# Optimization experiments

Hardware: AMD Instinct MI355X
Metric: run time of the kernel (lower is better)

Reference implementation:

```python
import jax, jax.numpy as jnp
import numpy as np

DIM = 1280
HEADS = 16
HEAD_DIM = DIM // HEADS  # 80
SEQ = 2048


def setup_inputs() -> dict:
    key = jax.random.key(0)
    ks = jax.random.split(key, 6)
    hidden_states = jax.random.normal(ks[0], (SEQ, DIM), jnp.float32)
    rotary_pos_emb = jax.random.normal(ks[1], (SEQ, HEAD_DIM // 2), jnp.float32)
    # 4 variable-length windows packed into one flat sequence
    cu_seqlens = jnp.array([0, 512, 1024, 1536, 2048], jnp.int32)
    w_scale = DIM ** -0.5
    qkv_w = jax.random.normal(ks[2], (3 * DIM, DIM), jnp.float32) * w_scale
    qkv_b = jax.random.normal(ks[3], (3 * DIM,), jnp.float32) * 0.01
    proj_w = jax.random.normal(ks[4], (DIM, DIM), jnp.float32) * w_scale
    proj_b = jax.random.normal(ks[5], (DIM,), jnp.float32) * 0.01
    return {
        "hidden_states": hidden_states,
        "rotary_pos_emb": rotary_pos_emb,
        "cu_seqlens": cu_seqlens,
        "qkv_w": qkv_w,
        "qkv_b": qkv_b,
        "proj_w": proj_w,
        "proj_b": proj_b,
    }


def _apply_rope_vision(x, freqs):
    # x: [S, H, D], freqs: [S, D//2]; matches Qwen2-VL apply_rotary_pos_emb_vision
    cos = jnp.concatenate([jnp.cos(freqs), jnp.cos(freqs)], axis=-1)[:, None, :]  # [S,1,D]
    sin = jnp.concatenate([jnp.sin(freqs), jnp.sin(freqs)], axis=-1)[:, None, :]
    x1, x2 = jnp.split(x, 2, axis=-1)
    rot = jnp.concatenate([-x2, x1], axis=-1)  # rotate_half
    return x * cos + rot * sin


def reference(hidden_states, rotary_pos_emb, cu_seqlens, qkv_w, qkv_b, proj_w, proj_b):
    S = hidden_states.shape[0]
    qkv = (hidden_states @ qkv_w.T + qkv_b).reshape(S, 3, HEADS, HEAD_DIM)
    q, k, v = qkv[:, 0], qkv[:, 1], qkv[:, 2]  # each [S, H, D]
    q = _apply_rope_vision(q, rotary_pos_emb)
    k = _apply_rope_vision(k, rotary_pos_emb)
    # varlen attention: tokens attend only within their cu_seqlens window
    seg = jnp.searchsorted(cu_seqlens[1:], jnp.arange(S), side="right")
    mask = seg[:, None] == seg[None, :]  # [S, S]
    scale = HEAD_DIM ** -0.5
    scores = jnp.einsum("shd,thd->hst", q, k) * scale  # [H, S, S]
    scores = jnp.where(mask[None, :, :], scores, jnp.finfo(scores.dtype).min)
    probs = jax.nn.softmax(scores, axis=-1)
    attn = jnp.einsum("hst,thd->shd", probs, v).reshape(S, DIM)
    return attn @ proj_w.T + proj_b
```

## Files before the change

kernel.cpp:

```cpp
#include <hip/hip_runtime.h>


typedef __attribute__((ext_vector_type(8))) short bf16x8;
typedef __attribute__((ext_vector_type(4))) float floatx4;
typedef __attribute__((ext_vector_type(4))) short short4v;
typedef __attribute__((ext_vector_type(8))) short short8v;

static __device__ __forceinline__ short f2bf(float f) {
  union { float f; unsigned u; } v; v.f = f;
  unsigned r = v.u + 0x7FFFu + ((v.u >> 16) & 1u);
  return (short)(r >> 16);
}
static __device__ __forceinline__ float bf2f(short h) {
  union { unsigned u; float f; } v;
  v.u = ((unsigned)(unsigned short)h) << 16;
  return v.f;
}

static __device__ __forceinline__ void gload16(const short* g, short* l) {
  __builtin_amdgcn_global_load_lds(
      (const __attribute__((address_space(1))) unsigned*)g,
      (__attribute__((address_space(3))) unsigned*)l, 16, 0, 0);
}

__global__ __launch_bounds__(256) void cvt_kernel(const float* __restrict__ src,
                                                  short* __restrict__ dst, int n8) {
  int i = blockIdx.x * 256 + threadIdx.x;
  if (i >= n8) return;
  float4 x = ((const float4*)src)[2 * i];
  float4 y = ((const float4*)src)[2 * i + 1];
  short8v o;
  o[0] = f2bf(x.x); o[1] = f2bf(x.y); o[2] = f2bf(x.z); o[3] = f2bf(x.w);
  o[4] = f2bf(y.x); o[5] = f2bf(y.y); o[6] = f2bf(y.z); o[7] = f2bf(y.w);
  ((short8v*)dst)[i] = o;
}

template <int MODE, int BM, int BN>
__global__ __launch_bounds__(256) void gemm_lds(const short* __restrict__ A,
                                                const short* __restrict__ B,
                                                const float* __restrict__ bias,
                                                void* __restrict__ Cout,
                                                short* __restrict__ vt,
                                                int M, int N, int K) {
  constexpr int AR = BM / 64;
  constexpr int BR = BN / 64;
  constexpr int MI = BM / 32;
  constexpr int NJ = BN / 32;
  __shared__ short As[BM * 32];
  __shared__ short Bs[BN * 32];

  const int tid = threadIdx.x;
  const int lane = tid & 63;
  const int wave = tid >> 6;
  const int l15 = lane & 15, quad = lane >> 4;

  const short* gA[AR]; short* lA[AR];
#pragma unroll
  for (int r = 0; r < AR; ++r) {
    int ch = r * 256 + tid;
    gA[r] = A + (size_t)(blockIdx.y * BM + (ch >> 2)) * K + (ch & 3) * 8;
    lA[r] = As + ch * 8;
  }
  const short* gB[BR]; short* lB[BR];
#pragma unroll
  for (int r = 0; r < BR; ++r) {
    int ch = r * 256 + tid;
    gB[r] = B + (size_t)(blockIdx.x * BN + (ch >> 2)) * K + (ch & 3) * 8;
    lB[r] = Bs + ch * 8;
  }

  const int wm = (wave >> 1) * (BM / 2);
  const int wn = (wave & 1) * (BN / 2);

  floatx4 acc[MI][NJ];
#pragma unroll
  for (int i = 0; i < MI; ++i)
#pragma unroll
    for (int j = 0; j < NJ; ++j) acc[i][j] = (floatx4){0.f, 0.f, 0.f, 0.f};

  for (int k0 = 0; k0 < K; k0 += 32) {
#pragma unroll
    for (int r = 0; r < AR; ++r) { gload16(gA[r], lA[r]); gA[r] += 32; }
#pragma unroll
    for (int r = 0; r < BR; ++r) { gload16(gB[r], lB[r]); gB[r] += 32; }
    __syncthreads();

    bf16x8 af[MI], bf[NJ];
#pragma unroll
    for (int i = 0; i < MI; ++i)
      af[i] = *(const bf16x8*)(As + (wm + i * 16 + l15) * 32 + quad * 8);
#pragma unroll
    for (int j = 0; j < NJ; ++j)
      bf[j] = *(const bf16x8*)(Bs + (wn + j * 16 + l15) * 32 + quad * 8);
#pragma unroll
    for (int i = 0; i < MI; ++i)
#pragma unroll
      for (int j = 0; j < NJ; ++j)
        acc[i][j] = __builtin_amdgcn_mfma_f32_16x16x32_bf16(af[i], bf[j], acc[i][j], 0, 0, 0);
    __syncthreads();
  }

  const int bm = blockIdx.y * BM + wm;
  const int bn = blockIdx.x * BN + wn;
#pragma unroll
  for (int j = 0; j < NJ; ++j) {
    const int col = bn + j * 16 + l15;
    const float bs = bias[col];
    if (MODE == 1) {
      float* C = (float*)Cout;
#pragma unroll
      for (int i = 0; i < MI; ++i) {
        const int row0 = bm + i * 16 + quad * 4;
#pragma unroll
        for (int e = 0; e < 4; ++e)
          C[(size_t)(row0 + e) * N + col] = acc[i][j][e] + bs;
      }
    } else {
      if (bn + j * 16 < 2560) {
        short* C = (short*)Cout;
#pragma unroll
        for (int i = 0; i < MI; ++i) {
          const int row0 = bm + i * 16 + quad * 4;
#pragma unroll
          for (int e = 0; e < 4; ++e)
            C[(size_t)(row0 + e) * 2560 + col] = f2bf(acc[i][j][e] + bs);
        }
      } else {
#pragma unroll
        for (int i = 0; i < MI; ++i) {
          const int row0 = bm + i * 16 + quad * 4;
          short4v v;
#pragma unroll
          for (int e = 0; e < 4; ++e) v[e] = f2bf(acc[i][j][e] + bs);
          *(short4v*)(vt + (size_t)(col - 2560) * 2048 + row0) = v;
        }
      }
    }
  }
}

__global__ __launch_bounds__(256) void rope_repack(const short* __restrict__ qkv,
                                                   const float* __restrict__ rot,
                                                   short* __restrict__ qp,
                                                   short* __restrict__ kp) {
  int idx = blockIdx.x * 256 + threadIdx.x;
  int d = idx % 96;
  int t = idx / 96;
  int s = t & 2047;
  int h = t >> 11;
  size_t dst = ((size_t)h * 2048 + s) * 96 + d;
  if (d < 80) {
    int base = s * 2560 + h * 80;
    int df = (d < 40) ? d : d - 40;
    int dp = (d < 40) ? d + 40 : d - 40;
    float fr = rot[s * 40 + df];
    float c = __cosf(fr), sn = __sinf(fr);
    float sgn = (d < 40) ? -1.f : 1.f;
    float xq = bf2f(qkv[base + d]);
    float pq = bf2f(qkv[base + dp]);
    float xk = bf2f(qkv[base + 1280 + d]);
    float pk = bf2f(qkv[base + 1280 + dp]);
    qp[dst] = f2bf((xq * c + sgn * pq * sn) * 0.11180339887498949f);
    kp[dst] = f2bf(xk * c + sgn * pk * sn);
  } else {
    qp[dst] = 0;
    kp[dst] = 0;
  }
}

__global__ __launch_bounds__(256) void attn_kernel(const short* __restrict__ qp,
                                                   const short* __restrict__ kp,
                                                   const short* __restrict__ vt,
                                                   short* __restrict__ attnout) {
  __shared__ short P[4][16][264];
  const int lane = threadIdx.x & 63;
  const int wave = threadIdx.x >> 6;
  const int l15 = lane & 15, quad = lane >> 4;
  const int g = blockIdx.x;
  const int head = g >> 5;
  const int seg = (g >> 3) & 3;
  const int grp = g & 7;
  const int q0 = seg * 512 + (grp * 4 + wave) * 16;

  const short* qb = qp + ((size_t)head * 2048 + q0 + l15) * 96 + quad * 8;
  bf16x8 aq0 = *(const bf16x8*)qb;
  bf16x8 aq1 = *(const bf16x8*)(qb + 32);
  bf16x8 aq2 = *(const bf16x8*)(qb + 64);

  floatx4 s[32];
  const short* kb0 = kp + ((size_t)head * 2048 + seg * 512 + l15) * 96 + quad * 8;
#pragma unroll
  for (int j = 0; j < 32; ++j) {
    const short* kb = kb0 + j * 16 * 96;
    floatx4 acc = (floatx4){0.f, 0.f, 0.f, 0.f};
    acc = __builtin_amdgcn_mfma_f32_16x16x32_bf16(aq0, *(const bf16x8*)kb, acc, 0, 0, 0);
    acc = __builtin_amdgcn_mfma_f32_16x16x32_bf16(aq1, *(const bf16x8*)(kb + 32), acc, 0, 0, 0);
    acc = __builtin_amdgcn_mfma_f32_16x16x32_bf16(aq2, *(const bf16x8*)(kb + 64), acc, 0, 0, 0);
    s[j] = acc;
  }

  float m[4] = {-1e30f, -1e30f, -1e30f, -1e30f};
#pragma unroll
  for (int j = 0; j < 32; ++j)
#pragma unroll
    for (int e = 0; e < 4; ++e) m[e] = fmaxf(m[e], s[j][e]);
#pragma unroll
  for (int e = 0; e < 4; ++e)
#pragma unroll
    for (int o = 1; o < 16; o <<= 1) m[e] = fmaxf(m[e], __shfl_xor(m[e], o));
  float l[4] = {0.f, 0.f, 0.f, 0.f};
#pragma unroll
  for (int j = 0; j < 32; ++j)
#pragma unroll
    for (int e = 0; e < 4; ++e) {
      float p = __expf(s[j][e] - m[e]);
      s[j][e] = p;
      l[e] += p;
    }
#pragma unroll
  for (int e = 0; e < 4; ++e)
#pragma unroll
    for (int o = 1; o < 16; o <<= 1) l[e] += __shfl_xor(l[e], o);
  float inv[4];
#pragma unroll
  for (int e = 0; e < 4; ++e) inv[e] = 1.f / l[e];

  floatx4 o5[5];
#pragma unroll
  for (int t = 0; t < 5; ++t) o5[t] = (floatx4){0.f, 0.f, 0.f, 0.f};
  const short* vb = vt + ((size_t)(head * 80 + l15)) * 2048 + seg * 512 + quad * 8;
#pragma unroll
  for (int half = 0; half < 2; ++half) {
#pragma unroll
    for (int j = 0; j < 16; ++j)
#pragma unroll
      for (int e = 0; e < 4; ++e)
        P[wave][quad * 4 + e][j * 16 + l15] = f2bf(s[half * 16 + j][e]);
#pragma unroll
    for (int kk = 0; kk < 8; ++kk) {
      bf16x8 ap = *(const bf16x8*)&P[wave][l15][kk * 32 + quad * 8];
#pragma unroll
      for (int t = 0; t < 5; ++t) {
        bf16x8 bv = *(const bf16x8*)(vb + (size_t)t * 16 * 2048 + half * 256 + kk * 32);
        o5[t] = __builtin_amdgcn_mfma_f32_16x16x32_bf16(ap, bv, o5[t], 0, 0, 0);
      }
    }
  }
#pragma unroll
  for (int t = 0; t < 5; ++t)
#pragma unroll
    for (int e = 0; e < 4; ++e)
      attnout[(size_t)(q0 + quad * 4 + e) * 1280 + head * 80 + t * 16 + l15] =
          f2bf(o5[t][e] * inv[e]);
}

extern "C" void kernel_launch(void* const* d_in, const int* in_sizes, int n_in,
                              void* d_out, int out_size, void* d_ws, size_t ws_size,
                              hipStream_t stream) {
  const float* hidden = (const float*)d_in[0];
  const float* rotary = (const float*)d_in[1];
  const float* qkv_w = (const float*)d_in[3];
  const float* qkv_b = (const float*)d_in[4];
  const float* proj_w = (const float*)d_in[5];
  const float* proj_b = (const float*)d_in[6];
  float* out = (float*)d_out;

  char* w = (char*)d_ws;
  short* hA   = (short*)(w + 0);
  short* w1   = (short*)(w + 5242880);
  short* w2   = (short*)(w + 15073280);
  short* qkvb = (short*)(w + 18350080);
  short* qp   = (short*)(w + 28835840);
  short* kp   = (short*)(w + 35127296);
  short* vt   = (short*)(w + 41418752);
  short* attn = (short*)(w + 46661632);

  cvt_kernel<<<1280, 256, 0, stream>>>(hidden, hA, 2621440 / 8);
  cvt_kernel<<<2400, 256, 0, stream>>>(qkv_w, w1, 4915200 / 8);
  cvt_kernel<<<800, 256, 0, stream>>>(proj_w, w2, 1638400 / 8);

  gemm_lds<2, 128, 128><<<dim3(3840 / 128, 2048 / 128), 256, 0, stream>>>(
      hA, w1, qkv_b, (void*)qkvb, vt, 2048, 3840, 1280);

  rope_repack<<<16 * 2048 * 96 / 256, 256, 0, stream>>>(qkvb, rotary, qp, kp);

  attn_kernel<<<512, 256, 0, stream>>>(qp, kp, vt, attn);

  gemm_lds<1, 128, 64><<<dim3(1280 / 64, 2048 / 128), 256, 0, stream>>>(
      attn, w2, proj_b, (void*)out, nullptr, 2048, 1280, 1280);
}
```

Before: 203.9 us.

## Stage K/V tiles in shared memory with double buffering; fuse convert kernels

The attention kernel now cooperatively loads 128-key chunks of K and V^T into double-buffered LDS using global_load_lds, so the four waves share each tile instead of each reading K/V from global memory on its own. The block-to-(head,segment) mapping is reordered so that consecutive blocks cover different head/segment pairs. The three fp32-to-bf16 conversion launches are merged into one kernel. The cost is extra block-level barriers and a larger LDS footprint, which may reduce occupancy.

```diff
diff --git a/kernel.cpp b/kernel.cpp
--- a/kernel.cpp
+++ b/kernel.cpp
@@ -23,16 +23,23 @@
       (__attribute__((address_space(3))) unsigned*)l, 16, 0, 0);
 }
 
-__global__ __launch_bounds__(256) void cvt_kernel(const float* __restrict__ src,
-                                                  short* __restrict__ dst, int n8) {
+#define CVT_N1 327680
+#define CVT_N2 614400
+#define CVT_N3 204800
+__global__ __launch_bounds__(256) void cvt3_kernel(const float* __restrict__ s1, short* __restrict__ d1,
+                                                   const float* __restrict__ s2, short* __restrict__ d2,
+                                                   const float* __restrict__ s3, short* __restrict__ d3) {
   int i = blockIdx.x * 256 + threadIdx.x;
-  if (i >= n8) return;
-  float4 x = ((const float4*)src)[2 * i];
-  float4 y = ((const float4*)src)[2 * i + 1];
+  const float* s; short* d; int j;
+  if (i < CVT_N1)                { s = s1; d = d1; j = i; }
+  else if (i < CVT_N1 + CVT_N2)  { s = s2; d = d2; j = i - CVT_N1; }
+  else                           { s = s3; d = d3; j = i - CVT_N1 - CVT_N2; }
+  float4 x = ((const float4*)s)[2 * j];
+  float4 y = ((const float4*)s)[2 * j + 1];
   short8v o;
   o[0] = f2bf(x.x); o[1] = f2bf(x.y); o[2] = f2bf(x.z); o[3] = f2bf(x.w);
   o[4] = f2bf(y.x); o[5] = f2bf(y.y); o[6] = f2bf(y.z); o[7] = f2bf(y.w);
-  ((short8v*)dst)[i] = o;
+  ((short8v*)d)[j] = o;
 }
 
 template <int MODE, int BM, int BN>
@@ -85,18 +92,18 @@
     for (int r = 0; r < BR; ++r) { gload16(gB[r], lB[r]); gB[r] += 32; }
     __syncthreads();
 
-    bf16x8 af[MI], bf[NJ];
+    bf16x8 af[MI], bfr[NJ];
 #pragma unroll
     for (int i = 0; i < MI; ++i)
       af[i] = *(const bf16x8*)(As + (wm + i * 16 + l15) * 32 + quad * 8);
 #pragma unroll
     for (int j = 0; j < NJ; ++j)
-      bf[j] = *(const bf16x8*)(Bs + (wn + j * 16 + l15) * 32 + quad * 8);
+      bfr[j] = *(const bf16x8*)(Bs + (wn + j * 16 + l15) * 32 + quad * 8);
 #pragma unroll
     for (int i = 0; i < MI; ++i)
 #pragma unroll
       for (int j = 0; j < NJ; ++j)
-        acc[i][j] = __builtin_amdgcn_mfma_f32_16x16x32_bf16(af[i], bf[j], acc[i][j], 0, 0, 0);
+        acc[i][j] = __builtin_amdgcn_mfma_f32_16x16x32_bf16(af[i], bfr[j], acc[i][j], 0, 0, 0);
     __syncthreads();
   }
 
@@ -172,14 +179,21 @@
                                                    const short* __restrict__ kp,
                                                    const short* __restrict__ vt,
                                                    short* __restrict__ attnout) {
-  __shared__ short P[4][16][264];
-  const int lane = threadIdx.x & 63;
-  const int wave = threadIdx.x >> 6;
+  __shared__ short smem[29184];
+  short* const Ks[2] = {smem, smem + 12288};
+  short* const Vs[2] = {smem, smem + 10240};
+
+  const int tid = threadIdx.x;
+  const int lane = tid & 63;
+  const int wave = tid >> 6;
   const int l15 = lane & 15, quad = lane >> 4;
+  short* const Pw = smem + 20480 + wave * (16 * 136);
+
   const int g = blockIdx.x;
-  const int head = g >> 5;
-  const int seg = (g >> 3) & 3;
-  const int grp = g & 7;
+  const int hs = g & 63;
+  const int grp = g >> 6;
+  const int head = hs >> 2;
+  const int seg = hs & 3;
   const int q0 = seg * 512 + (grp * 4 + wave) * 16;
 
   const short* qb = qp + ((size_t)head * 2048 + q0 + l15) * 96 + quad * 8;
@@ -187,16 +201,38 @@
   bf16x8 aq1 = *(const bf16x8*)(qb + 32);
   bf16x8 aq2 = *(const bf16x8*)(qb + 64);
 
+  const short* kbase = kp + ((size_t)head * 2048 + seg * 512) * 96;
+  const short* vbase = vt + (size_t)head * 80 * 2048 + seg * 512;
+
   floatx4 s[32];
-  const short* kb0 = kp + ((size_t)head * 2048 + seg * 512 + l15) * 96 + quad * 8;
-#pragma unroll
-  for (int j = 0; j < 32; ++j) {
-    const short* kb = kb0 + j * 16 * 96;
-    floatx4 acc = (floatx4){0.f, 0.f, 0.f, 0.f};
-    acc = __builtin_amdgcn_mfma_f32_16x16x32_bf16(aq0, *(const bf16x8*)kb, acc, 0, 0, 0);
-    acc = __builtin_amdgcn_mfma_f32_16x16x32_bf16(aq1, *(const bf16x8*)(kb + 32), acc, 0, 0, 0);
-    acc = __builtin_amdgcn_mfma_f32_16x16x32_bf16(aq2, *(const bf16x8*)(kb + 64), acc, 0, 0, 0);
-    s[j] = acc;
+  {
+#pragma unroll
+    for (int r = 0; r < 6; ++r) {
+      int idx = r * 256 + tid;
+      gload16(kbase + idx * 8, Ks[0] + idx * 8);
+    }
+#pragma unroll
+    for (int c = 0; c < 4; ++c) {
+      __syncthreads();
+      if (c < 3) {
+        const short* src = kbase + (size_t)(c + 1) * 128 * 96;
+#pragma unroll
+        for (int r = 0; r < 6; ++r) {
+          int idx = r * 256 + tid;
+          gload16(src + idx * 8, Ks[(c + 1) & 1] + idx * 8);
+        }
+      }
+      const short* kl = Ks[c & 1];
+#pragma unroll
+      for (int j = 0; j < 8; ++j) {
+        const short* kb = kl + (j * 16 + l15) * 96 + quad * 8;
+        floatx4 acc = (floatx4){0.f, 0.f, 0.f, 0.f};
+        acc = __builtin_amdgcn_mfma_f32_16x16x32_bf16(aq0, *(const bf16x8*)kb, acc, 0, 0, 0);
+        acc = __builtin_amdgcn_mfma_f32_16x16x32_bf16(aq1, *(const bf16x8*)(kb + 32), acc, 0, 0, 0);
+        acc = __builtin_amdgcn_mfma_f32_16x16x32_bf16(aq2, *(const bf16x8*)(kb + 64), acc, 0, 0, 0);
+        s[c * 8 + j] = acc;
+      }
+    }
   }
 
   float m[4] = {-1e30f, -1e30f, -1e30f, -1e30f};
@@ -228,24 +264,41 @@
   floatx4 o5[5];
 #pragma unroll
   for (int t = 0; t < 5; ++t) o5[t] = (floatx4){0.f, 0.f, 0.f, 0.f};
-  const short* vb = vt + ((size_t)(head * 80 + l15)) * 2048 + seg * 512 + quad * 8;
-#pragma unroll
-  for (int half = 0; half < 2; ++half) {
-#pragma unroll
-    for (int j = 0; j < 16; ++j)
+
+  __syncthreads();
+#pragma unroll
+  for (int r = 0; r < 5; ++r) {
+    int idx = r * 256 + tid;
+    gload16(vbase + (size_t)(idx >> 4) * 2048 + (idx & 15) * 8, Vs[0] + idx * 8);
+  }
+#pragma unroll
+  for (int c = 0; c < 4; ++c) {
+    __syncthreads();
+    if (c < 3) {
+      const short* src = vbase + (c + 1) * 128;
+#pragma unroll
+      for (int r = 0; r < 5; ++r) {
+        int idx = r * 256 + tid;
+        gload16(src + (size_t)(idx >> 4) * 2048 + (idx & 15) * 8, Vs[(c + 1) & 1] + idx * 8);
+      }
+    }
+#pragma unroll
+    for (int j = 0; j < 8; ++j)
 #pragma unroll
       for (int e = 0; e < 4; ++e)
-        P[wave][quad * 4 + e][j * 16 + l15] = f2bf(s[half * 16 + j][e]);
-#pragma unroll
-    for (int kk = 0; kk < 8; ++kk) {
-      bf16x8 ap = *(const bf16x8*)&P[wave][l15][kk * 32 + quad * 8];
+        Pw[(quad * 4 + e) * 136 + j * 16 + l15] = f2bf(s[c * 8 + j][e]);
+    const short* vl = Vs[c & 1];
+#pragma unroll
+    for (int kk = 0; kk < 4; ++kk) {
+      bf16x8 ap = *(const bf16x8*)&Pw[l15 * 136 + kk * 32 + quad * 8];
 #pragma unroll
       for (int t = 0; t < 5; ++t) {
-        bf16x8 bv = *(const bf16x8*)(vb + (size_t)t * 16 * 2048 + half * 256 + kk * 32);
+        bf16x8 bv = *(const bf16x8*)&vl[(t * 16 + l15) * 128 + kk * 32 + quad * 8];
         o5[t] = __builtin_amdgcn_mfma_f32_16x16x32_bf16(ap, bv, o5[t], 0, 0, 0);
       }
     }
   }
+
 #pragma unroll
   for (int t = 0; t < 5; ++t)
 #pragma unroll
@@ -275,9 +328,7 @@
   short* vt   = (short*)(w + 41418752);
   short* attn = (short*)(w + 46661632);
 
-  cvt_kernel<<<1280, 256, 0, stream>>>(hidden, hA, 2621440 / 8);
-  cvt_kernel<<<2400, 256, 0, stream>>>(qkv_w, w1, 4915200 / 8);
-  cvt_kernel<<<800, 256, 0, stream>>>(proj_w, w2, 1638400 / 8);
+  cvt3_kernel<<<4480, 256, 0, stream>>>(hidden, hA, qkv_w, w1, proj_w, w2);
 
   gemm_lds<2, 128, 128><<<dim3(3840 / 128, 2048 / 128), 256, 0, stream>>>(
       hA, w1, qkv_b, (void*)qkvb, vt, 2048, 3840, 1280);
```

Result: faster. 186.8 us (-8.4%).
